# Kernel tuning notes

Measured on AMD Instinct MI355X. Metric: run time of the kernel, lower is better.

The kernel has to match this reference:

```python
import jax, jax.numpy as jnp
import numpy as np

NUM_USERS = 100000
NUM_ITEMS = 50000
D = 64
NUM_LAYERS = 2
NNZ_H = 3200000
NNZ_I = 3000000
EPS = 1e-12


def setup_inputs() -> dict:
    key = jax.random.key(0)
    ks = jax.random.split(key, 24)
    inp = {}
    inp['user_emb'] = jax.random.normal(ks[0], (NUM_USERS, D), jnp.float32) * 0.1
    inp['item_emb'] = jax.random.normal(ks[1], (NUM_ITEMS, D), jnp.float32) * 0.1
    inp['gating_w'] = jax.random.normal(ks[2], (4, D, D), jnp.float32) * 0.1
    inp['gating_b'] = jax.random.normal(ks[3], (4, 1, D), jnp.float32) * 0.1
    inp['sgating_w'] = jax.random.normal(ks[4], (3, D, D), jnp.float32) * 0.1
    inp['sgating_b'] = jax.random.normal(ks[5], (3, 1, D), jnp.float32) * 0.1
    inp['att_mat'] = jax.random.normal(ks[6], (D, D), jnp.float32) * 0.1
    inp['att_agg'] = jax.random.normal(ks[7], (1, D), jnp.float32) * 0.1
    inp['hs_row'] = jax.random.randint(ks[8], (NNZ_H,), 0, NUM_USERS, jnp.int32)
    inp['hs_col'] = jax.random.randint(ks[9], (NNZ_H,), 0, NUM_USERS, jnp.int32)
    inp['hs_val'] = jax.random.uniform(ks[10], (NNZ_H,), jnp.float32) / 32.0
    inp['hj_row'] = jax.random.randint(ks[11], (NNZ_H,), 0, NUM_USERS, jnp.int32)
    inp['hj_col'] = jax.random.randint(ks[12], (NNZ_H,), 0, NUM_USERS, jnp.int32)
    inp['hj_val'] = jax.random.uniform(ks[13], (NNZ_H,), jnp.float32) / 32.0
    inp['hp_row'] = jax.random.randint(ks[14], (NNZ_H,), 0, NUM_USERS, jnp.int32)
    inp['hp_col'] = jax.random.randint(ks[15], (NNZ_H,), 0, NUM_USERS, jnp.int32)
    inp['hp_val'] = jax.random.uniform(ks[16], (NNZ_H,), jnp.float32) / 32.0
    inp['inter_row'] = jax.random.randint(ks[17], (NNZ_I,), 0, NUM_USERS, jnp.int32)
    inp['inter_col'] = jax.random.randint(ks[18], (NNZ_I,), 0, NUM_ITEMS, jnp.int32)
    inp['inter_val'] = jax.random.uniform(ks[19], (NNZ_I,), jnp.float32) / 32.0
    return inp


def spmm(row, col, val, x, n_rows):
    # sparse (n_rows x m) @ dense (m x d), COO edges
    return jax.ops.segment_sum(val[:, None] * x[col], row, num_segments=n_rows)


def l2norm(x):
    return x / jnp.maximum(jnp.linalg.norm(x, axis=1, keepdims=True), EPS)


def self_gating(em, w, b):
    return em * jax.nn.sigmoid(em @ w + b)


def channel_attention(embs, att_mat, att_agg):
    # embs: list of 3 arrays [N, D]
    w = jnp.stack([jnp.sum(att_agg * (e @ att_mat), axis=1) for e in embs])  # [3, N]
    score = jax.nn.softmax(w, axis=0)
    mixed = score[0][:, None] * embs[0] + score[1][:, None] * embs[1] + score[2][:, None] * embs[2]
    return mixed, score


def reference(user_emb, item_emb, gating_w, gating_b, sgating_w, sgating_b,
              att_mat, att_agg,
              hs_row, hs_col, hs_val, hj_row, hj_col, hj_val,
              hp_row, hp_col, hp_val, inter_row, inter_col, inter_val):
    u_c0 = self_gating(user_emb, gating_w[0], gating_b[0])
    u_c1 = self_gating(user_emb, gating_w[1], gating_b[1])
    u_c2 = self_gating(user_emb, gating_w[2], gating_b[2])
    u_simple = self_gating(user_emb, gating_w[3], gating_b[3])
    it = item_emb
    acc_c0, acc_c1, acc_c2 = u_c0, u_c1, u_c2
    acc_simple, acc_item = u_simple, it
    for _ in range(NUM_LAYERS):
        mixed, _ = channel_attention([u_c0, u_c1, u_c2], att_mat, att_agg)
        mixed = (mixed + u_simple) / 2.0
        u_c0 = spmm(hs_row, hs_col, hs_val, u_c0, NUM_USERS)
        acc_c0 = acc_c0 + l2norm(u_c0)
        u_c1 = spmm(hj_row, hj_col, hj_val, u_c1, NUM_USERS)
        acc_c1 = acc_c1 + l2norm(u_c1)
        u_c2 = spmm(hp_row, hp_col, hp_val, u_c2, NUM_USERS)
        acc_c2 = acc_c2 + l2norm(u_c2)
        new_item = spmm(inter_col, inter_row, inter_val, mixed, NUM_ITEMS)  # inter^T @ mixed
        acc_item = acc_item + l2norm(new_item)
        u_simple = spmm(inter_row, inter_col, inter_val, it, NUM_USERS)  # inter @ item (old)
        acc_simple = acc_simple + l2norm(u_simple)
        it = new_item
    final_user, _ = channel_attention([acc_c0, acc_c1, acc_c2], att_mat, att_agg)
    final_user = final_user + acc_simple / 2.0
    sg0 = self_gating(final_user, sgating_w[0], sgating_b[0])
    sg1 = self_gating(final_user, sgating_w[1], sgating_b[1])
    sg2 = self_gating(final_user, sgating_w[2], sgating_b[2])
    return final_user, acc_item, sg0, sg1, sg2
```

## Files before the change

### kernel.cpp

```cpp
#include <hip/hip_runtime.h>

#define D 64
#define EPS 1e-12f

#define SB 6
#define BSZ (1 << SB)
#define NBMAX 2048
#define NCHUNK 128

__device__ __forceinline__ float wave_sum(float v) {
#pragma unroll
  for (int off = 32; off > 0; off >>= 1) v += __shfl_xor(v, off, 64);
  return v;
}

__global__ void compute_v_kernel(const float* __restrict__ att_mat,
                                 const float* __restrict__ att_agg,
                                 float* __restrict__ v) {
  int d = threadIdx.x;
  float s = 0.f;
#pragma unroll
  for (int j = 0; j < D; ++j) s += att_mat[d * D + j] * att_agg[j];
  v[d] = s;
}

__global__ __launch_bounds__(256) void gating4_kernel(
    const float* __restrict__ emb, const float* __restrict__ W,
    const float* __restrict__ B, float* __restrict__ u0, float* __restrict__ u1,
    float* __restrict__ u2, float* __restrict__ u3, float* __restrict__ a0,
    float* __restrict__ a1, float* __restrict__ a2, float* __restrict__ a3,
    int nrows) {
  __shared__ float4 sW4[D * D];
  for (int i = threadIdx.x; i < D * D; i += blockDim.x)
    sW4[i] = make_float4(W[i], W[D * D + i], W[2 * D * D + i],
                         W[3 * D * D + i]);
  __syncthreads();
  int lane = threadIdx.x & 63;
  int wid = (blockIdx.x * blockDim.x + threadIdx.x) >> 6;
  int nw = (gridDim.x * blockDim.x) >> 6;
  float b0 = B[0 * D + lane], b1 = B[1 * D + lane];
  float b2 = B[2 * D + lane], b3 = B[3 * D + lane];
  for (int r0 = wid * 4; r0 < nrows; r0 += nw * 4) {
    float e[4];
    float y[4][4];
#pragma unroll
    for (int i = 0; i < 4; ++i) {
      int r = r0 + i < nrows ? r0 + i : r0;
      e[i] = emb[(size_t)r * D + lane];
      y[i][0] = b0; y[i][1] = b1; y[i][2] = b2; y[i][3] = b3;
    }
#pragma unroll 16
    for (int j = 0; j < D; ++j) {
      float4 w = sW4[j * D + lane];
#pragma unroll
      for (int i = 0; i < 4; ++i) {
        float ej = __shfl(e[i], j, 64);
        y[i][0] += ej * w.x;
        y[i][1] += ej * w.y;
        y[i][2] += ej * w.z;
        y[i][3] += ej * w.w;
      }
    }
#pragma unroll
    for (int i = 0; i < 4; ++i) {
      int r = r0 + i;
      if (r < nrows) {
        size_t idx = (size_t)r * D + lane;
        float o0 = e[i] / (1.f + __expf(-y[i][0]));
        float o1 = e[i] / (1.f + __expf(-y[i][1]));
        float o2 = e[i] / (1.f + __expf(-y[i][2]));
        float o3 = e[i] / (1.f + __expf(-y[i][3]));
        u0[idx] = o0; u1[idx] = o1; u2[idx] = o2; u3[idx] = o3;
        if (a0) { a0[idx] = o0; a1[idx] = o1; a2[idx] = o2; a3[idx] = o3; }
      }
    }
  }
}

__global__ __launch_bounds__(256) void sgating3_kernel(
    const float* __restrict__ x, const float* __restrict__ W,
    const float* __restrict__ B, float* __restrict__ o0f,
    float* __restrict__ o1f, float* __restrict__ o2f, int nrows) {
  __shared__ float4 sW4[D * D];
  for (int i = threadIdx.x; i < D * D; i += blockDim.x)
    sW4[i] = make_float4(W[i], W[D * D + i], W[2 * D * D + i], 0.f);
  __syncthreads();
  int lane = threadIdx.x & 63;
  int wid = (blockIdx.x * blockDim.x + threadIdx.x) >> 6;
  int nw = (gridDim.x * blockDim.x) >> 6;
  float b0 = B[0 * D + lane], b1 = B[1 * D + lane], b2 = B[2 * D + lane];
  for (int r0 = wid * 4; r0 < nrows; r0 += nw * 4) {
    float e[4];
    float y[4][3];
#pragma unroll
    for (int i = 0; i < 4; ++i) {
      int r = r0 + i < nrows ? r0 + i : r0;
      e[i] = x[(size_t)r * D + lane];
      y[i][0] = b0; y[i][1] = b1; y[i][2] = b2;
    }
#pragma unroll 16
    for (int j = 0; j < D; ++j) {
      float4 w = sW4[j * D + lane];
#pragma unroll
      for (int i = 0; i < 4; ++i) {
        float ej = __shfl(e[i], j, 64);
        y[i][0] += ej * w.x;
        y[i][1] += ej * w.y;
        y[i][2] += ej * w.z;
      }
    }
#pragma unroll
    for (int i = 0; i < 4; ++i) {
      int r = r0 + i;
      if (r < nrows) {
        size_t idx = (size_t)r * D + lane;
        o0f[idx] = e[i] / (1.f + __expf(-y[i][0]));
        o1f[idx] = e[i] / (1.f + __expf(-y[i][1]));
        o2f[idx] = e[i] / (1.f + __expf(-y[i][2]));
      }
    }
  }
}

__global__ __launch_bounds__(256) void attn_mix_kernel(
    const float* __restrict__ u0, const float* __restrict__ u1,
    const float* __restrict__ u2, const float* __restrict__ us,
    const float* __restrict__ v, float* __restrict__ mixed, int nrows) {
  int lane = threadIdx.x & 63;
  int wid = (blockIdx.x * blockDim.x + threadIdx.x) >> 6;
  if (wid >= nrows) return;
  int idx = wid * D + lane;
  float e0 = u0[idx], e1 = u1[idx], e2 = u2[idx], eu = us[idx];
  float vd = v[lane];
  float w0 = wave_sum(e0 * vd);
  float w1 = wave_sum(e1 * vd);
  float w2 = wave_sum(e2 * vd);
  float m = fmaxf(w0, fmaxf(w1, w2));
  float s0 = __expf(w0 - m), s1 = __expf(w1 - m), s2 = __expf(w2 - m);
  float inv = 1.f / (s0 + s1 + s2);
  mixed[idx] = ((s0 * e0 + s1 * e1 + s2 * e2) * inv + eu) * 0.5f;
}

__global__ __launch_bounds__(256) void final_attn_kernel(
    const float* __restrict__ a0, const float* __restrict__ a1,
    const float* __restrict__ a2, const float* __restrict__ as,
    const float* __restrict__ v, float* __restrict__ out, int nrows) {
  int lane = threadIdx.x & 63;
  int wid = (blockIdx.x * blockDim.x + threadIdx.x) >> 6;
  if (wid >= nrows) return;
  int idx = wid * D + lane;
  float e0 = a0[idx], e1 = a1[idx], e2 = a2[idx], eu = as[idx];
  float vd = v[lane];
  float w0 = wave_sum(e0 * vd);
  float w1 = wave_sum(e1 * vd);
  float w2 = wave_sum(e2 * vd);
  float m = fmaxf(w0, fmaxf(w1, w2));
  float s0 = __expf(w0 - m), s1 = __expf(w1 - m), s2 = __expf(w2 - m);
  float inv = 1.f / (s0 + s1 + s2);
  out[idx] = (s0 * e0 + s1 * e1 + s2 * e2) * inv + 0.5f * eu;
}

__global__ __launch_bounds__(256) void l2acc_kernel(const float* __restrict__ x,
                                                    float* __restrict__ acc,
                                                    int nrows) {
  int lane = threadIdx.x & 63;
  int wid = (blockIdx.x * blockDim.x + threadIdx.x) >> 6;
  if (wid >= nrows) return;
  int idx = wid * D + lane;
  float xv = x[idx];
  float ss = wave_sum(xv * xv);
  float nrm = fmaxf(sqrtf(ss), EPS);
  acc[idx] += xv / nrm;
}

__global__ __launch_bounds__(256) void spmm_atomic_kernel(
    const int* __restrict__ row, const int* __restrict__ col,
    const float* __restrict__ val, const float* __restrict__ x,
    float* __restrict__ out, int nnz) {
  int lane = threadIdx.x & 63;
  int wid = (blockIdx.x * blockDim.x + threadIdx.x) >> 6;
  int nw = (gridDim.x * blockDim.x) >> 6;
  for (int base = wid * 64; base < nnz; base += nw * 64) {
    int e = base + lane;
    int r = 0, c = 0;
    float v = 0.f;
    if (e < nnz) { r = row[e]; c = col[e]; v = val[e]; }
    int cnt = nnz - base; if (cnt > 64) cnt = 64;
    for (int i = 0; i < cnt; ++i) {
      int ri = __shfl(r, i, 64);
      int ci = __shfl(c, i, 64);
      float vi = __shfl(v, i, 64);
      float xv = x[ci * D + lane];
      atomicAdd(&out[ri * D + lane], vi * xv);
    }
  }
}


__global__ __launch_bounds__(256) void hist_kernel(const int* __restrict__ row,
                                                   int* __restrict__ counts,
                                                   int nnz) {
  int i = blockIdx.x * blockDim.x + threadIdx.x;
  int n = gridDim.x * blockDim.x;
  for (; i < nnz; i += n) atomicAdd(&counts[row[i]], 1);
}

__global__ __launch_bounds__(256) void scan1_kernel(const int* __restrict__ in,
                                                    int* __restrict__ out,
                                                    int* __restrict__ partials,
                                                    int n) {
  __shared__ int lds[256];
  int t = threadIdx.x;
  int base = blockIdx.x * 2048 + t * 8;
  int v[8];
  int s = 0;
#pragma unroll
  for (int k = 0; k < 8; ++k) {
    int i = base + k;
    v[k] = (i < n) ? in[i] : 0;
    s += v[k];
  }
  lds[t] = s;
  __syncthreads();
  for (int ofs = 1; ofs < 256; ofs <<= 1) {
    int add = 0;
    if (t >= ofs) add = lds[t - ofs];
    __syncthreads();
    if (t >= ofs) lds[t] += add;
    __syncthreads();
  }
  int excl = lds[t] - s;
  if (t == 255) partials[blockIdx.x] = lds[255];
  int run = excl;
#pragma unroll
  for (int k = 0; k < 8; ++k) {
    int i = base + k;
    if (i < n) out[i] = run;
    run += v[k];
  }
}

__global__ __launch_bounds__(256) void scan2_kernel(int* __restrict__ partials,
                                                    int P) {
  __shared__ int lds[256];
  int t = threadIdx.x;
  int s = (t < P) ? partials[t] : 0;
  lds[t] = s;
  __syncthreads();
  for (int ofs = 1; ofs < 256; ofs <<= 1) {
    int add = 0;
    if (t >= ofs) add = lds[t - ofs];
    __syncthreads();
    if (t >= ofs) lds[t] += add;
    __syncthreads();
  }
  if (t < P) partials[t] = lds[t] - s;
}

__global__ __launch_bounds__(256) void scan3_kernel(
    int* __restrict__ out, const int* __restrict__ partials, int n) {
  int i = blockIdx.x * blockDim.x + threadIdx.x;
  int nt = gridDim.x * blockDim.x;
  for (; i < n; i += nt) out[i] += partials[i >> 11];
}

__global__ __launch_bounds__(256) void bhist_kernel(
    const int* __restrict__ row, int* __restrict__ bh, int nnz, int nb,
    int chunk) {
  __shared__ int hist[NBMAX];
  for (int i = threadIdx.x; i < nb; i += blockDim.x) hist[i] = 0;
  __syncthreads();
  int base = blockIdx.x * chunk;
  int lim = base + chunk;
  if (lim > nnz) lim = nnz;
  for (int e = base + threadIdx.x; e < lim; e += blockDim.x)
    atomicAdd(&hist[row[e] >> SB], 1);
  __syncthreads();
  int* o = bh + blockIdx.x * nb;
  for (int i = threadIdx.x; i < nb; i += blockDim.x) o[i] = hist[i];
}

__global__ __launch_bounds__(256) void bscan_kernel(
    const int* __restrict__ row_ptr, int* __restrict__ bh, int nb) {
  int b = blockIdx.x * blockDim.x + threadIdx.x;
  if (b >= nb) return;
  int run = row_ptr[b << SB];
#pragma unroll 4
  for (int k = 0; k < NCHUNK; ++k) {
    int idx = k * nb + b;
    int t = bh[idx];
    bh[idx] = run;
    run += t;
  }
}

__global__ __launch_bounds__(256) void bscatter_kernel(
    const int* __restrict__ row, const int* __restrict__ col,
    const float* __restrict__ val, const int* __restrict__ bh,
    int2* __restrict__ staging, int nnz, int nb, int chunk) {
  __shared__ int cur[NBMAX];
  const int* o = bh + blockIdx.x * nb;
  for (int i = threadIdx.x; i < nb; i += blockDim.x) cur[i] = o[i];
  __syncthreads();
  int base = blockIdx.x * chunk;
  int lim = base + chunk;
  if (lim > nnz) lim = nnz;
  for (int e = base + threadIdx.x; e < lim; e += blockDim.x) {
    int r = row[e];
    int b = r >> SB;
    int idx = atomicAdd(&cur[b], 1);
    staging[idx] =
        make_int2(((r & (BSZ - 1)) << 24) | col[e], __float_as_int(val[e]));
  }
}

__global__ __launch_bounds__(256) void bucket_scatter_kernel(
    const int* __restrict__ row_ptr, const int2* __restrict__ staging,
    int2* __restrict__ edges_out, int nrows) {
  __shared__ int lfill[BSZ];
  int b = blockIdx.x;
  int r0 = b << SB;
  int t = threadIdx.x;
  int rend = r0 + BSZ;
  if (rend > nrows) rend = nrows;
  if (t < BSZ) {
    int r = r0 + t;
    lfill[t] = row_ptr[r < nrows ? r : nrows];
  }
  int bstart = row_ptr[r0];
  int bend = row_ptr[rend];
  __syncthreads();
  for (int e = bstart + t; e < bend; e += blockDim.x) {
    int2 ev = staging[e];
    int lrow = ((unsigned)ev.x) >> 24;
    int idx = atomicAdd(&lfill[lrow], 1);
    edges_out[idx] = make_int2(ev.x & 0xFFFFFF, ev.y);
  }
}

__global__ __launch_bounds__(256) void spmm_csr_l2acc_kernel(
    const int* __restrict__ row_ptr, const int2* __restrict__ edges,
    const float* __restrict__ x, float* __restrict__ out,
    float* __restrict__ acc, const float* __restrict__ init, int nrows) {
  int lane = threadIdx.x & 63;
  int r = (blockIdx.x * blockDim.x + threadIdx.x) >> 6;
  if (r >= nrows) return;
  int start = row_ptr[r], end = row_ptr[r + 1];
  float sum = 0.f;
  for (int j = start; j < end; j += 64) {
    int e = j + lane;
    int c = 0;
    float v = 0.f;
    if (e < end) {
      int2 ev = edges[e];
      c = ev.x;
      v = __int_as_float(ev.y);
    }
    int cnt = end - j;
    if (cnt > 64) cnt = 64;
    int i = 0;
    for (; i + 4 <= cnt; i += 4) {
      int c0 = __shfl(c, i, 64);
      int c1 = __shfl(c, i + 1, 64);
      int c2 = __shfl(c, i + 2, 64);
      int c3 = __shfl(c, i + 3, 64);
      float v0 = __shfl(v, i, 64);
      float v1 = __shfl(v, i + 1, 64);
      float v2 = __shfl(v, i + 2, 64);
      float v3 = __shfl(v, i + 3, 64);
      float x0 = x[c0 * D + lane];
      float x1 = x[c1 * D + lane];
      float x2 = x[c2 * D + lane];
      float x3 = x[c3 * D + lane];
      sum += v0 * x0;
      sum += v1 * x1;
      sum += v2 * x2;
      sum += v3 * x3;
    }
    for (; i < cnt; ++i) {
      int ci = __shfl(c, i, 64);
      float vi = __shfl(v, i, 64);
      sum += vi * x[ci * D + lane];
    }
  }
  int idx = r * D + lane;
  out[idx] = sum;
  float ss = wave_sum(sum * sum);
  float nrm = fmaxf(sqrtf(ss), EPS);
  float base = init ? init[idx] : acc[idx];
  acc[idx] = base + sum / nrm;
}


static void build_csr(const int* row, const int* col, const float* val, int nnz,
                      int nrows, int* counts, int* row_ptr, int* partials,
                      int* bh, int2* staging, int2* edges_out,
                      hipStream_t stream) {
  int n1 = nrows + 1;
  hipMemsetAsync(counts, 0, n1 * sizeof(int), stream);
  hipLaunchKernelGGL(hist_kernel, dim3(1024), dim3(256), 0, stream, row, counts,
                     nnz);
  int nblk = (n1 + 2047) / 2048;
  hipLaunchKernelGGL(scan1_kernel, dim3(nblk), dim3(256), 0, stream, counts,
                     row_ptr, partials, n1);
  hipLaunchKernelGGL(scan2_kernel, dim3(1), dim3(256), 0, stream, partials,
                     nblk);
  hipLaunchKernelGGL(scan3_kernel, dim3(64), dim3(256), 0, stream, row_ptr,
                     partials, n1);
  int nb = (nrows + BSZ - 1) >> SB;
  int chunk = (nnz + NCHUNK - 1) / NCHUNK;
  hipLaunchKernelGGL(bhist_kernel, dim3(NCHUNK), dim3(256), 0, stream, row, bh,
                     nnz, nb, chunk);
  hipLaunchKernelGGL(bscan_kernel, dim3((nb + 255) / 256), dim3(256), 0, stream,
                     row_ptr, bh, nb);
  hipLaunchKernelGGL(bscatter_kernel, dim3(NCHUNK), dim3(256), 0, stream, row,
                     col, val, bh, staging, nnz, nb, chunk);
  hipLaunchKernelGGL(bucket_scatter_kernel, dim3(nb), dim3(256), 0, stream,
                     row_ptr, staging, edges_out, nrows);
}

extern "C" void kernel_launch(void* const* d_in, const int* in_sizes, int n_in,
                              void* d_out, int out_size, void* d_ws,
                              size_t ws_size, hipStream_t stream) {
  const float* user_emb = (const float*)d_in[0];
  const float* item_emb = (const float*)d_in[1];
  const float* gating_w = (const float*)d_in[2];
  const float* gating_b = (const float*)d_in[3];
  const float* sgating_w = (const float*)d_in[4];
  const float* sgating_b = (const float*)d_in[5];
  const float* att_mat = (const float*)d_in[6];
  const float* att_agg = (const float*)d_in[7];
  const int* hs_row = (const int*)d_in[8];
  const int* hs_col = (const int*)d_in[9];
  const float* hs_val = (const float*)d_in[10];
  const int* hj_row = (const int*)d_in[11];
  const int* hj_col = (const int*)d_in[12];
  const float* hj_val = (const float*)d_in[13];
  const int* hp_row = (const int*)d_in[14];
  const int* hp_col = (const int*)d_in[15];
  const float* hp_val = (const float*)d_in[16];
  const int* inter_row = (const int*)d_in[17];
  const int* inter_col = (const int*)d_in[18];
  const float* inter_val = (const float*)d_in[19];

  const int U = in_sizes[0] / D;
  const int I = in_sizes[1] / D;
  const int NH = in_sizes[8];
  const int NI = in_sizes[17];
  const size_t UD = (size_t)U * D;
  const size_t ID = (size_t)I * D;

  float* out = (float*)d_out;
  float* final_user = out;
  float* acc_item = out + UD;
  float* sg0 = out + UD + ID;
  float* sg1 = sg0 + UD;
  float* sg2 = sg1 + UD;
  float* acc0 = sg0, *acc1 = sg1, *acc2 = sg2, *accS = final_user;

  char* p = (char*)d_ws;
  auto alloc = [&](size_t bytes) -> void* {
    void* r = (void*)p;
    p += (bytes + 255) & ~(size_t)255;
    return r;
  };
  float* u0 = (float*)alloc(UD * 4);
  float* u1 = (float*)alloc(UD * 4);
  float* u2 = (float*)alloc(UD * 4);
  float* us = (float*)alloc(UD * 4);
  float* mixed = (float*)alloc(UD * 4);
  float* spare = (float*)alloc(UD * 4);
  float* it_a = (float*)alloc(ID * 4);
  float* it_b = (float*)alloc(ID * 4);
  float* v = (float*)alloc(256 * 4);
  int* partials = (int*)alloc(256 * 4);
  int* cnt_u = (int*)alloc((U + 2) * 4);
  int* cnt_i = (int*)alloc((I + 2) * 4);
  int* bh = (int*)alloc((size_t)NCHUNK * NBMAX * 4);
  int* rp_hs = (int*)alloc((U + 2) * 4);
  int* rp_hj = (int*)alloc((U + 2) * 4);
  int* rp_hp = (int*)alloc((U + 2) * 4);
  int* rp_iu = (int*)alloc((U + 2) * 4);
  int* rp_ii = (int*)alloc((I + 2) * 4);
  size_t NMAX = (size_t)(NH > NI ? NH : NI);
  int2* staging;
  if (NMAX * 8 <= UD * 4) staging = (int2*)spare;
  else staging = (int2*)alloc(NMAX * 8);
  int2* ed_hs = (int2*)alloc((size_t)NH * 8);
  int2* ed_hj = (int2*)alloc((size_t)NH * 8);
  int2* ed_hp = (int2*)alloc((size_t)NH * 8);
  int2* ed_iu = (int2*)alloc((size_t)NI * 8);
  int2* ed_ii = (int2*)alloc((size_t)NI * 8);
  size_t needed = (size_t)(p - (char*)d_ws);
  bool use_csr = needed <= ws_size && U < (1 << 24) && I < (1 << 24) &&
                 U <= NBMAX * BSZ && I <= NBMAX * BSZ;

  const int ROWB_U = (U + 3) / 4;
  const int ROWB_I = (I + 3) / 4;
  const int SPMM_BLOCKS = 2048;

  hipLaunchKernelGGL(compute_v_kernel, dim3(1), dim3(64), 0, stream, att_mat,
                     att_agg, v);
  hipLaunchKernelGGL(gating4_kernel, dim3(512), dim3(256), 0, stream, user_emb,
                     gating_w, gating_b, u0, u1, u2, us,
                     use_csr ? (float*)nullptr : acc0,
                     use_csr ? (float*)nullptr : acc1,
                     use_csr ? (float*)nullptr : acc2,
                     use_csr ? (float*)nullptr : accS, U);
  if (!use_csr) {
    hipMemcpyAsync(acc_item, item_emb, ID * sizeof(float),
                   hipMemcpyDeviceToDevice, stream);
    hipMemcpyAsync(it_a, item_emb, ID * sizeof(float), hipMemcpyDeviceToDevice,
                   stream);
  }

  if (use_csr) {
    build_csr(hs_row, hs_col, hs_val, NH, U, cnt_u, rp_hs, partials, bh,
              staging, ed_hs, stream);
    build_csr(hj_row, hj_col, hj_val, NH, U, cnt_u, rp_hj, partials, bh,
              staging, ed_hj, stream);
    build_csr(hp_row, hp_col, hp_val, NH, U, cnt_u, rp_hp, partials, bh,
              staging, ed_hp, stream);
    build_csr(inter_row, inter_col, inter_val, NI, U, cnt_u, rp_iu, partials,
              bh, staging, ed_iu, stream);
    build_csr(inter_col, inter_row, inter_val, NI, I, cnt_i, rp_ii, partials,
              bh, staging, ed_ii, stream);
  }

  const float* it_src = item_emb;
  float* it_dst = it_b;
  float* it_old = it_a;
  float* it_new = it_b;

  for (int layer = 0; layer < 2; ++layer) {
    hipLaunchKernelGGL(attn_mix_kernel, dim3(ROWB_U), dim3(256), 0, stream, u0,
                       u1, u2, us, v, mixed, U);
    if (use_csr) {
      const float* i0 = (layer == 0) ? u0 : nullptr;
      const float* i1 = (layer == 0) ? u1 : nullptr;
      const float* i2 = (layer == 0) ? u2 : nullptr;
      const float* ii = (layer == 0) ? item_emb : nullptr;
      const float* is = (layer == 0) ? us : nullptr;
      hipLaunchKernelGGL(spmm_csr_l2acc_kernel, dim3(ROWB_U), dim3(256), 0,
                         stream, rp_hs, ed_hs, u0, spare, acc0, i0, U);
      { float* t = u0; u0 = spare; spare = t; }
      hipLaunchKernelGGL(spmm_csr_l2acc_kernel, dim3(ROWB_U), dim3(256), 0,
                         stream, rp_hj, ed_hj, u1, spare, acc1, i1, U);
      { float* t = u1; u1 = spare; spare = t; }
      hipLaunchKernelGGL(spmm_csr_l2acc_kernel, dim3(ROWB_U), dim3(256), 0,
                         stream, rp_hp, ed_hp, u2, spare, acc2, i2, U);
      { float* t = u2; u2 = spare; spare = t; }
      hipLaunchKernelGGL(spmm_csr_l2acc_kernel, dim3(ROWB_I), dim3(256), 0,
                         stream, rp_ii, ed_ii, mixed, it_dst, acc_item, ii, I);
      hipLaunchKernelGGL(spmm_csr_l2acc_kernel, dim3(ROWB_U), dim3(256), 0,
                         stream, rp_iu, ed_iu, it_src, spare, accS, is, U);
      { float* t = us; us = spare; spare = t; }
      it_src = it_dst;
      it_dst = it_a;
    } else {
      hipMemsetAsync(spare, 0, UD * sizeof(float), stream);
      hipLaunchKernelGGL(spmm_atomic_kernel, dim3(SPMM_BLOCKS), dim3(256), 0,
                         stream, hs_row, hs_col, hs_val, u0, spare, NH);
      hipLaunchKernelGGL(l2acc_kernel, dim3(ROWB_U), dim3(256), 0, stream,
                         spare, acc0, U);
      { float* t = u0; u0 = spare; spare = t; }
      hipMemsetAsync(spare, 0, UD * sizeof(float), stream);
      hipLaunchKernelGGL(spmm_atomic_kernel, dim3(SPMM_BLOCKS), dim3(256), 0,
                         stream, hj_row, hj_col, hj_val, u1, spare, NH);
      hipLaunchKernelGGL(l2acc_kernel, dim3(ROWB_U), dim3(256), 0, stream,
                         spare, acc1, U);
      { float* t = u1; u1 = spare; spare = t; }
      hipMemsetAsync(spare, 0, UD * sizeof(float), stream);
      hipLaunchKernelGGL(spmm_atomic_kernel, dim3(SPMM_BLOCKS), dim3(256), 0,
                         stream, hp_row, hp_col, hp_val, u2, spare, NH);
      hipLaunchKernelGGL(l2acc_kernel, dim3(ROWB_U), dim3(256), 0, stream,
                         spare, acc2, U);
      { float* t = u2; u2 = spare; spare = t; }
      hipMemsetAsync(it_new, 0, ID * sizeof(float), stream);
      hipLaunchKernelGGL(spmm_atomic_kernel, dim3(SPMM_BLOCKS), dim3(256), 0,
                         stream, inter_col, inter_row, inter_val, mixed, it_new,
                         NI);
      hipLaunchKernelGGL(l2acc_kernel, dim3(ROWB_I), dim3(256), 0, stream,
                         it_new, acc_item, I);
      hipMemsetAsync(spare, 0, UD * sizeof(float), stream);
      hipLaunchKernelGGL(spmm_atomic_kernel, dim3(SPMM_BLOCKS), dim3(256), 0,
                         stream, inter_row, inter_col, inter_val, it_old, spare,
                         NI);
      hipLaunchKernelGGL(l2acc_kernel, dim3(ROWB_U), dim3(256), 0, stream,
                         spare, accS, U);
      { float* t = us; us = spare; spare = t; }
      { float* t = it_old; it_old = it_new; it_new = t; }
    }
  }

  hipLaunchKernelGGL(final_attn_kernel, dim3(ROWB_U), dim3(256), 0, stream,
                     acc0, acc1, acc2, accS, v, final_user, U);
  hipLaunchKernelGGL(sgating3_kernel, dim3(512), dim3(256), 0, stream,
                     final_user, sgating_w, sgating_b, sg0, sg1, sg2, U);
}
```

Baseline: 3.281 ms.

## Make bucketed CSR build chunk-major so each chunk writes a contiguous staging region

The CSR construction used to lay out staging bucket-major, with a column-wise scan over chunks for each bucket. Now each chunk scans its own bucket histogram and writes into its own contiguous staging region. A gather kernel per bucket then reads that bucket's fragment from each of the 128 chunks and places edges into their final rows. The aim is to replace the strided, serial bscan and to make the scatter writes more local. The cost is that the gather kernel now reads 128 small fragments per bucket, which may not be coalesced well.

```diff
diff --git a/kernel.cpp b/kernel.cpp
--- a/kernel.cpp
+++ b/kernel.cpp
@@ -276,30 +276,52 @@
   for (int e = base + threadIdx.x; e < lim; e += blockDim.x)
     atomicAdd(&hist[row[e] >> SB], 1);
   __syncthreads();
-  int* o = bh + blockIdx.x * nb;
+  int* o = bh + (size_t)blockIdx.x * nb;
   for (int i = threadIdx.x; i < nb; i += blockDim.x) o[i] = hist[i];
 }
 
-__global__ __launch_bounds__(256) void bscan_kernel(
-    const int* __restrict__ row_ptr, int* __restrict__ bh, int nb) {
-  int b = blockIdx.x * blockDim.x + threadIdx.x;
-  if (b >= nb) return;
-  int run = row_ptr[b << SB];
-#pragma unroll 4
-  for (int k = 0; k < NCHUNK; ++k) {
-    int idx = k * nb + b;
-    int t = bh[idx];
-    bh[idx] = run;
-    run += t;
-  }
-}
-
-__global__ __launch_bounds__(256) void bscatter_kernel(
+__global__ __launch_bounds__(256) void chunkscan_kernel(
+    const int* __restrict__ bh, int* __restrict__ fo, int nnz, int nb,
+    int chunk) {
+  __shared__ int lds[256];
+  int k = blockIdx.x;
+  int base = k * chunk;
+  int t = threadIdx.x;
+  const int* in = bh + (size_t)k * nb;
+  int v[8];
+  int s = 0;
+#pragma unroll
+  for (int q = 0; q < 8; ++q) {
+    int b = t * 8 + q;
+    v[q] = (b < nb) ? in[b] : 0;
+    s += v[q];
+  }
+  lds[t] = s;
+  __syncthreads();
+  for (int ofs = 1; ofs < 256; ofs <<= 1) {
+    int add = 0;
+    if (t >= ofs) add = lds[t - ofs];
+    __syncthreads();
+    if (t >= ofs) lds[t] += add;
+    __syncthreads();
+  }
+  int run = base + lds[t] - s;
+  int* o = fo + (size_t)k * (nb + 1);
+#pragma unroll
+  for (int q = 0; q < 8; ++q) {
+    int b = t * 8 + q;
+    if (b < nb) o[b] = run;
+    run += v[q];
+  }
+  if (t == 255) o[nb] = run;
+}
+
+__global__ __launch_bounds__(256) void bscatter2_kernel(
     const int* __restrict__ row, const int* __restrict__ col,
-    const float* __restrict__ val, const int* __restrict__ bh,
+    const float* __restrict__ val, const int* __restrict__ fo,
     int2* __restrict__ staging, int nnz, int nb, int chunk) {
   __shared__ int cur[NBMAX];
-  const int* o = bh + blockIdx.x * nb;
+  const int* o = fo + (size_t)blockIdx.x * (nb + 1);
   for (int i = threadIdx.x; i < nb; i += blockDim.x) cur[i] = o[i];
   __syncthreads();
   int base = blockIdx.x * chunk;
@@ -314,27 +336,33 @@
   }
 }
 
-__global__ __launch_bounds__(256) void bucket_scatter_kernel(
-    const int* __restrict__ row_ptr, const int2* __restrict__ staging,
-    int2* __restrict__ edges_out, int nrows) {
+__global__ __launch_bounds__(256) void bucket_gather_kernel(
+    const int* __restrict__ row_ptr, const int* __restrict__ fo,
+    const int2* __restrict__ staging, int2* __restrict__ edges_out, int nrows,
+    int nb) {
   __shared__ int lfill[BSZ];
+  __shared__ int2 sfrag[NCHUNK];
   int b = blockIdx.x;
-  int r0 = b << SB;
   int t = threadIdx.x;
-  int rend = r0 + BSZ;
-  if (rend > nrows) rend = nrows;
   if (t < BSZ) {
-    int r = r0 + t;
+    int r = (b << SB) + t;
     lfill[t] = row_ptr[r < nrows ? r : nrows];
   }
-  int bstart = row_ptr[r0];
-  int bend = row_ptr[rend];
-  __syncthreads();
-  for (int e = bstart + t; e < bend; e += blockDim.x) {
-    int2 ev = staging[e];
-    int lrow = ((unsigned)ev.x) >> 24;
-    int idx = atomicAdd(&lfill[lrow], 1);
-    edges_out[idx] = make_int2(ev.x & 0xFFFFFF, ev.y);
+  if (t < NCHUNK) {
+    const int* o = fo + (size_t)t * (nb + 1) + b;
+    sfrag[t] = make_int2(o[0], o[1]);
+  }
+  __syncthreads();
+  int lane = t & 63;
+  int w = t >> 6;
+  for (int k = w; k < NCHUNK; k += 4) {
+    int2 f = sfrag[k];
+    for (int e = f.x + lane; e < f.y; e += 64) {
+      int2 ev = staging[e];
+      int lrow = ((unsigned)ev.x) >> 24;
+      int idx = atomicAdd(&lfill[lrow], 1);
+      edges_out[idx] = make_int2(ev.x & 0xFFFFFF, ev.y);
+    }
   }
 }
 
@@ -394,7 +422,7 @@
 
 static void build_csr(const int* row, const int* col, const float* val, int nnz,
                       int nrows, int* counts, int* row_ptr, int* partials,
-                      int* bh, int2* staging, int2* edges_out,
+                      int* bh, int* fo, int2* staging, int2* edges_out,
                       hipStream_t stream) {
   int n1 = nrows + 1;
   hipMemsetAsync(counts, 0, n1 * sizeof(int), stream);
@@ -411,12 +439,12 @@
   int chunk = (nnz + NCHUNK - 1) / NCHUNK;
   hipLaunchKernelGGL(bhist_kernel, dim3(NCHUNK), dim3(256), 0, stream, row, bh,
                      nnz, nb, chunk);
-  hipLaunchKernelGGL(bscan_kernel, dim3((nb + 255) / 256), dim3(256), 0, stream,
-                     row_ptr, bh, nb);
-  hipLaunchKernelGGL(bscatter_kernel, dim3(NCHUNK), dim3(256), 0, stream, row,
-                     col, val, bh, staging, nnz, nb, chunk);
-  hipLaunchKernelGGL(bucket_scatter_kernel, dim3(nb), dim3(256), 0, stream,
-                     row_ptr, staging, edges_out, nrows);
+  hipLaunchKernelGGL(chunkscan_kernel, dim3(NCHUNK), dim3(256), 0, stream, bh,
+                     fo, nnz, nb, chunk);
+  hipLaunchKernelGGL(bscatter2_kernel, dim3(NCHUNK), dim3(256), 0, stream, row,
+                     col, val, fo, staging, nnz, nb, chunk);
+  hipLaunchKernelGGL(bucket_gather_kernel, dim3(nb), dim3(256), 0, stream,
+                     row_ptr, fo, staging, edges_out, nrows, nb);
 }
 
 extern "C" void kernel_launch(void* const* d_in, const int* in_sizes, int n_in,
@@ -477,6 +505,7 @@
   int* cnt_u = (int*)alloc((U + 2) * 4);
   int* cnt_i = (int*)alloc((I + 2) * 4);
   int* bh = (int*)alloc((size_t)NCHUNK * NBMAX * 4);
+  int* fo = (int*)alloc((size_t)NCHUNK * (NBMAX + 1) * 4);
   int* rp_hs = (int*)alloc((U + 2) * 4);
   int* rp_hj = (int*)alloc((U + 2) * 4);
   int* rp_hp = (int*)alloc((U + 2) * 4);
@@ -515,16 +544,16 @@
   }
 
   if (use_csr) {
-    build_csr(hs_row, hs_col, hs_val, NH, U, cnt_u, rp_hs, partials, bh,
+    build_csr(hs_row, hs_col, hs_val, NH, U, cnt_u, rp_hs, partials, bh, fo,
               staging, ed_hs, stream);
-    build_csr(hj_row, hj_col, hj_val, NH, U, cnt_u, rp_hj, partials, bh,
+    build_csr(hj_row, hj_col, hj_val, NH, U, cnt_u, rp_hj, partials, bh, fo,
               staging, ed_hj, stream);
-    build_csr(hp_row, hp_col, hp_val, NH, U, cnt_u, rp_hp, partials, bh,
+    build_csr(hp_row, hp_col, hp_val, NH, U, cnt_u, rp_hp, partials, bh, fo,
               staging, ed_hp, stream);
     build_csr(inter_row, inter_col, inter_val, NI, U, cnt_u, rp_iu, partials,
-              bh, staging, ed_iu, stream);
+              bh, fo, staging, ed_iu, stream);
     build_csr(inter_col, inter_row, inter_val, NI, I, cnt_i, rp_ii, partials,
-              bh, staging, ed_ii, stream);
+              bh, fo, staging, ed_ii, stream);
   }
 
   const float* it_src = item_emb;
```

Result: faster. 3.216 ms (-2.0%).
